# Kernel optimization log

Measured on AMD Instinct MI355X. Metric: run time of the kernel, lower is better.

Reference implementation:

```python
import jax, jax.numpy as jnp
import numpy as np

MARGIN = 0.3
EPS = 1e-12


def setup_inputs() -> dict:
    key = jax.random.key(0)
    k1, k2 = jax.random.split(key)
    inputs = jax.random.normal(k1, (256, 2048), dtype=jnp.float32)
    targets = jax.random.randint(k2, (256,), 0, 32, dtype=jnp.int64)
    return {"inputs": inputs, "targets": targets}


def reference(inputs, targets):
    # Pairwise Euclidean distance matrix [n, n] via GEMM.
    sq = jnp.sum(inputs * inputs, axis=1)                      # [n]
    dist = sq[:, None] + sq[None, :] - 2.0 * (inputs @ inputs.T)
    dist = jnp.sqrt(jnp.clip(dist, EPS, None))                 # [n, n]

    same = targets[:, None] == targets[None, :]                # [n, n]
    # Triplet margin for all (anchor, positive, negative) in one broadcast.
    tri = dist[:, :, None] - dist[:, None, :] + MARGIN         # [n, n, n]
    tri = jnp.clip(tri, EPS, None)
    # Valid: same label for (a, p), different label for (a, neg).
    valid = same[:, :, None] & (~same)[:, None, :]             # [n, n, n]
    # Torch version stacks only valid triplets (dynamic shape); here we
    # return the dense [n, n, n] tensor with invalid entries zeroed.
    return jnp.where(valid, tri, 0.0)
```

## Files before the change

### kernel.cpp

```cpp
#include <hip/hip_runtime.h>
#include <hip/hip_fp16.h>

#define N 256
#define D 2048
#define MARGIN_F 0.3f
#define EPS_F 1e-12f

typedef float v4f __attribute__((ext_vector_type(4)));

__global__ __launch_bounds__(64) void sq_kernel(const float* __restrict__ x,
                                                float* __restrict__ sq) {
    int row = blockIdx.x;
    int lane = threadIdx.x;
    const float4* xr = (const float4*)(x + (size_t)row * D);
    float acc = 0.f;
#pragma unroll
    for (int it = 0; it < 8; ++it) {
        float4 v = xr[lane + 64 * it];
        acc += v.x * v.x + v.y * v.y + v.z * v.z + v.w * v.w;
    }
#pragma unroll
    for (int off = 32; off > 0; off >>= 1) acc += __shfl_down(acc, off, 64);
    if (lane == 0) sq[row] = acc;
}

__global__ __launch_bounds__(256, 1) void gram_kernel(const float* __restrict__ x,
                                                      __half* __restrict__ part) {
    __shared__ __align__(16) float As[128 * 32];
    __shared__ __align__(16) float Bs[128 * 32];
    const int bi = blockIdx.x, bj = blockIdx.y, ks = blockIdx.z;
    const int i0 = bi * 128, j0 = bj * 128, k0 = ks * 32;
    const int tid = threadIdx.x;

#pragma unroll
    for (int it = 0; it < 4; ++it) {
        int f = tid + 256 * it;
        int row = f >> 3;
        int c4 = f & 7;
        int sc4 = c4 ^ ((row >> 3) & 7);
        float4 va = *(const float4*)(x + (size_t)(i0 + row) * D + k0 + c4 * 4);
        float4 vb = *(const float4*)(x + (size_t)(j0 + row) * D + k0 + c4 * 4);
        *(float4*)(As + row * 32 + sc4 * 4) = va;
        *(float4*)(Bs + row * 32 + sc4 * 4) = vb;
    }
    __syncthreads();

    const int tx = tid & 15;
    const int ty = tid >> 4;
    float acc[8][8];
#pragma unroll
    for (int r = 0; r < 8; ++r)
#pragma unroll
        for (int c = 0; c < 8; ++c) acc[r][c] = 0.f;

#pragma unroll
    for (int k4 = 0; k4 < 8; ++k4) {
        float4 a[8], b[8];
#pragma unroll
        for (int r = 0; r < 8; ++r) {
            int ia = ty * 8 + r;
            int ib = tx * 8 + r;
            a[r] = *(const float4*)(As + ia * 32 + ((k4 ^ ((ia >> 3) & 7)) << 2));
            b[r] = *(const float4*)(Bs + ib * 32 + ((k4 ^ ((ib >> 3) & 7)) << 2));
        }
#pragma unroll
        for (int r = 0; r < 8; ++r)
#pragma unroll
            for (int c = 0; c < 8; ++c)
                acc[r][c] += a[r].x * b[c].x + a[r].y * b[c].y +
                             a[r].z * b[c].z + a[r].w * b[c].w;
    }

    __half* pout = part + (size_t)ks * (N * N);
#pragma unroll
    for (int r = 0; r < 8; ++r) {
        int gi = i0 + ty * 8 + r;
        union { __half2 h2[4]; uint4 u; } pk;
#pragma unroll
        for (int c = 0; c < 4; ++c)
            pk.h2[c] = __floats2half2_rn(acc[r][2 * c], acc[r][2 * c + 1]);
        *(uint4*)(pout + (size_t)gi * N + j0 + tx * 8) = pk.u;
    }
}

__global__ __launch_bounds__(256) void fused_kernel(const __half* __restrict__ part,
                                                    const float* __restrict__ sq,
                                                    const int* __restrict__ targets,
                                                    float* __restrict__ out) {
    __shared__ __align__(16) float drow[N];
    __shared__ int lab[N];
    const int a = blockIdx.x;
    const int tid = threadIdx.x;
    lab[tid] = targets[tid];

    float dot = 0.f;
    const __half* base = part + a * N + tid;
#pragma unroll 8
    for (int ks = 0; ks < 64; ++ks)
        dot += __half2float(base[(size_t)ks * (N * N)]);
    drow[tid] = sqrtf(fmaxf(sq[a] + sq[tid] - 2.f * dot, EPS_F));
    __syncthreads();

    const int la = lab[a];
    const int lane = tid & 63;
    const int pq = tid >> 6;
    const int p0 = blockIdx.y * 128 + pq * 32;

    v4f dan = *(const v4f*)(drow + lane * 4);
    v4f mb = MARGIN_F - dan;
    v4f nokv = {(lab[lane * 4 + 0] != la) ? 1.f : 0.f,
                (lab[lane * 4 + 1] != la) ? 1.f : 0.f,
                (lab[lane * 4 + 2] != la) ? 1.f : 0.f,
                (lab[lane * 4 + 3] != la) ? 1.f : 0.f};

    float* obase = out + ((size_t)a << 16) + lane * 4;
#pragma unroll 4
    for (int i = 0; i < 32; ++i) {
        int p = p0 + i;
        v4f r = {0.f, 0.f, 0.f, 0.f};
        if (lab[p] == la) {
            float dap = drow[p];
            v4f t = dap + mb;
            t.x = fmaxf(t.x, EPS_F);
            t.y = fmaxf(t.y, EPS_F);
            t.z = fmaxf(t.z, EPS_F);
            t.w = fmaxf(t.w, EPS_F);
            r = t * nokv;
        }
        __builtin_nontemporal_store(r, (v4f*)(obase + (size_t)p * N));
    }
}

__global__ __launch_bounds__(256) void dist_kernel(const __half* __restrict__ part,
                                                   const float* __restrict__ sq,
                                                   float* __restrict__ dist) {
    const int a = blockIdx.x;
    const int tid = threadIdx.x;
    float dot = 0.f;
    const __half* base = part + a * N + tid;
#pragma unroll 8
    for (int ks = 0; ks < 64; ++ks)
        dot += __half2float(base[(size_t)ks * (N * N)]);
    dist[a * N + tid] = sqrtf(fmaxf(sq[a] + sq[tid] - 2.f * dot, EPS_F));
}

__global__ __launch_bounds__(256) void triplet_kernel(const float* __restrict__ dist,
                                                      const int* __restrict__ targets,
                                                      float* __restrict__ out) {
    __shared__ __align__(16) float drow[N];
    __shared__ int lab[N];
    const int a = blockIdx.x;
    const int p0 = blockIdx.y * 16;
    const int tid = threadIdx.x;
    lab[tid] = targets[tid];
    drow[tid] = dist[a * N + tid];
    __syncthreads();

    const int la = lab[a];
    const int lane = tid & 63;
    const int pq = tid >> 6;

    v4f dan = *(const v4f*)(drow + lane * 4);
    v4f mb = MARGIN_F - dan;
    v4f nokv = {(lab[lane * 4 + 0] != la) ? 1.f : 0.f,
                (lab[lane * 4 + 1] != la) ? 1.f : 0.f,
                (lab[lane * 4 + 2] != la) ? 1.f : 0.f,
                (lab[lane * 4 + 3] != la) ? 1.f : 0.f};

    float* obase = out + ((size_t)a << 16) + lane * 4;
#pragma unroll
    for (int j = 0; j < 4; ++j) {
        int p = p0 + pq * 4 + j;
        v4f r = {0.f, 0.f, 0.f, 0.f};
        if (lab[p] == la) {
            float dap = drow[p];
            v4f t = dap + mb;
            t.x = fmaxf(t.x, EPS_F);
            t.y = fmaxf(t.y, EPS_F);
            t.z = fmaxf(t.z, EPS_F);
            t.w = fmaxf(t.w, EPS_F);
            r = t * nokv;
        }
        __builtin_nontemporal_store(r, (v4f*)(obase + (size_t)p * N));
    }
}

extern "C" void kernel_launch(void* const* d_in, const int* in_sizes, int n_in,
                              void* d_out, int out_size, void* d_ws, size_t ws_size,
                              hipStream_t stream) {
    const float* x = (const float*)d_in[0];
    const int* targets = (const int*)d_in[1];
    float* out = (float*)d_out;
    float* ws = (float*)d_ws;

    float* sq = ws;
    size_t need_full = 1024 + (size_t)64 * N * N * sizeof(__half) + 1024;

    if (ws_size >= need_full) {
        __half* part = (__half*)(ws + 256);
        sq_kernel<<<256, 64, 0, stream>>>(x, sq);
        gram_kernel<<<dim3(2, 2, 64), 256, 0, stream>>>(x, part);
        fused_kernel<<<dim3(256, 2), 256, 0, stream>>>(part, sq, targets, out);
    } else {
        __half* part = (__half*)d_out;
        float* dist = ws + 256;
        sq_kernel<<<256, 64, 0, stream>>>(x, sq);
        gram_kernel<<<dim3(2, 2, 64), 256, 0, stream>>>(x, part);
        dist_kernel<<<256, 256, 0, stream>>>(part, sq, dist);
        triplet_kernel<<<dim3(256, 16), 256, 0, stream>>>(dist, targets, out);
    }
}
```

Before: 95.65 us.

## Retile Gram GEMM to 64x64x64 blocks with 32-way split-K and exact diagonal

The Gram kernel moves from 128x128 output tiles with 32-wide K slices over 64 splits to 64x64 tiles with 64-wide K slices over 32 splits. Shared memory uses a padded stride of 68 with an XOR swizzle, and each thread now holds a 4x4 accumulator instead of 8x8. This raises the block count to 512 and halves the fp16 partial-sum buffer, so the reduction reads half as many partials. The diagonal distance is also fixed to sqrt(eps) to avoid fp16 cancellation error, which is a correctness tweak.

```diff
diff --git a/kernel.cpp b/kernel.cpp
--- a/kernel.cpp
+++ b/kernel.cpp
@@ -5,6 +5,7 @@
 #define D 2048
 #define MARGIN_F 0.3f
 #define EPS_F 1e-12f
+#define SQRT_EPS_F 1e-6f
 
 typedef float v4f __attribute__((ext_vector_type(4)));
 
@@ -24,62 +25,60 @@
     if (lane == 0) sq[row] = acc;
 }
 
-__global__ __launch_bounds__(256, 1) void gram_kernel(const float* __restrict__ x,
-                                                      __half* __restrict__ part) {
-    __shared__ __align__(16) float As[128 * 32];
-    __shared__ __align__(16) float Bs[128 * 32];
-    const int bi = blockIdx.x, bj = blockIdx.y, ks = blockIdx.z;
-    const int i0 = bi * 128, j0 = bj * 128, k0 = ks * 32;
+__global__ __launch_bounds__(256) void gram_kernel(const float* __restrict__ x,
+                                                   __half* __restrict__ part) {
+    __shared__ __align__(16) float As[64 * 68];
+    __shared__ __align__(16) float Bs[64 * 68];
+    const int i0 = blockIdx.x * 64, j0 = blockIdx.y * 64, k0 = blockIdx.z * 64;
     const int tid = threadIdx.x;
 
 #pragma unroll
     for (int it = 0; it < 4; ++it) {
         int f = tid + 256 * it;
-        int row = f >> 3;
-        int c4 = f & 7;
-        int sc4 = c4 ^ ((row >> 3) & 7);
+        int row = f >> 4;
+        int c4 = f & 15;
+        int sc4 = c4 ^ ((row >> 2) & 15);
         float4 va = *(const float4*)(x + (size_t)(i0 + row) * D + k0 + c4 * 4);
         float4 vb = *(const float4*)(x + (size_t)(j0 + row) * D + k0 + c4 * 4);
-        *(float4*)(As + row * 32 + sc4 * 4) = va;
-        *(float4*)(Bs + row * 32 + sc4 * 4) = vb;
+        *(float4*)(As + row * 68 + sc4 * 4) = va;
+        *(float4*)(Bs + row * 68 + sc4 * 4) = vb;
     }
     __syncthreads();
 
     const int tx = tid & 15;
     const int ty = tid >> 4;
-    float acc[8][8];
-#pragma unroll
-    for (int r = 0; r < 8; ++r)
-#pragma unroll
-        for (int c = 0; c < 8; ++c) acc[r][c] = 0.f;
-
-#pragma unroll
-    for (int k4 = 0; k4 < 8; ++k4) {
-        float4 a[8], b[8];
-#pragma unroll
-        for (int r = 0; r < 8; ++r) {
-            int ia = ty * 8 + r;
-            int ib = tx * 8 + r;
-            a[r] = *(const float4*)(As + ia * 32 + ((k4 ^ ((ia >> 3) & 7)) << 2));
-            b[r] = *(const float4*)(Bs + ib * 32 + ((k4 ^ ((ib >> 3) & 7)) << 2));
+    float acc[4][4];
+#pragma unroll
+    for (int r = 0; r < 4; ++r)
+#pragma unroll
+        for (int c = 0; c < 4; ++c) acc[r][c] = 0.f;
+
+#pragma unroll
+    for (int k4 = 0; k4 < 16; ++k4) {
+        float4 a[4], b[4];
+        const int ca = (k4 ^ ty) << 2;
+        const int cb = (k4 ^ tx) << 2;
+#pragma unroll
+        for (int r = 0; r < 4; ++r) {
+            a[r] = *(const float4*)(As + (ty * 4 + r) * 68 + ca);
+            b[r] = *(const float4*)(Bs + (tx * 4 + r) * 68 + cb);
         }
 #pragma unroll
-        for (int r = 0; r < 8; ++r)
-#pragma unroll
-            for (int c = 0; c < 8; ++c)
+        for (int r = 0; r < 4; ++r)
+#pragma unroll
+            for (int c = 0; c < 4; ++c)
                 acc[r][c] += a[r].x * b[c].x + a[r].y * b[c].y +
                              a[r].z * b[c].z + a[r].w * b[c].w;
     }
 
-    __half* pout = part + (size_t)ks * (N * N);
-#pragma unroll
-    for (int r = 0; r < 8; ++r) {
-        int gi = i0 + ty * 8 + r;
-        union { __half2 h2[4]; uint4 u; } pk;
-#pragma unroll
-        for (int c = 0; c < 4; ++c)
-            pk.h2[c] = __floats2half2_rn(acc[r][2 * c], acc[r][2 * c + 1]);
-        *(uint4*)(pout + (size_t)gi * N + j0 + tx * 8) = pk.u;
+    __half* pout = part + (size_t)blockIdx.z * (N * N);
+#pragma unroll
+    for (int r = 0; r < 4; ++r) {
+        int gi = i0 + ty * 4 + r;
+        union { __half2 h2[2]; uint2 u; } pk;
+        pk.h2[0] = __floats2half2_rn(acc[r][0], acc[r][1]);
+        pk.h2[1] = __floats2half2_rn(acc[r][2], acc[r][3]);
+        *(uint2*)(pout + (size_t)gi * N + j0 + tx * 4) = pk.u;
     }
 }
 
@@ -96,9 +95,10 @@
     float dot = 0.f;
     const __half* base = part + a * N + tid;
 #pragma unroll 8
-    for (int ks = 0; ks < 64; ++ks)
+    for (int ks = 0; ks < 32; ++ks)
         dot += __half2float(base[(size_t)ks * (N * N)]);
-    drow[tid] = sqrtf(fmaxf(sq[a] + sq[tid] - 2.f * dot, EPS_F));
+    drow[tid] = (tid == a) ? SQRT_EPS_F
+                           : sqrtf(fmaxf(sq[a] + sq[tid] - 2.f * dot, EPS_F));
     __syncthreads();
 
     const int la = lab[a];
@@ -139,9 +139,10 @@
     float dot = 0.f;
     const __half* base = part + a * N + tid;
 #pragma unroll 8
-    for (int ks = 0; ks < 64; ++ks)
+    for (int ks = 0; ks < 32; ++ks)
         dot += __half2float(base[(size_t)ks * (N * N)]);
-    dist[a * N + tid] = sqrtf(fmaxf(sq[a] + sq[tid] - 2.f * dot, EPS_F));
+    dist[a * N + tid] = (tid == a) ? SQRT_EPS_F
+                                   : sqrtf(fmaxf(sq[a] + sq[tid] - 2.f * dot, EPS_F));
 }
 
 __global__ __launch_bounds__(256) void triplet_kernel(const float* __restrict__ dist,
@@ -194,18 +195,18 @@
     float* ws = (float*)d_ws;
 
     float* sq = ws;
-    size_t need_full = 1024 + (size_t)64 * N * N * sizeof(__half) + 1024;
+    size_t need_full = 1024 + (size_t)32 * N * N * sizeof(__half) + 1024;
 
     if (ws_size >= need_full) {
         __half* part = (__half*)(ws + 256);
         sq_kernel<<<256, 64, 0, stream>>>(x, sq);
-        gram_kernel<<<dim3(2, 2, 64), 256, 0, stream>>>(x, part);
+        gram_kernel<<<dim3(4, 4, 32), 256, 0, stream>>>(x, part);
         fused_kernel<<<dim3(256, 2), 256, 0, stream>>>(part, sq, targets, out);
     } else {
         __half* part = (__half*)d_out;
         float* dist = ws + 256;
         sq_kernel<<<256, 64, 0, stream>>>(x, sq);
-        gram_kernel<<<dim3(2, 2, 64), 256, 0, stream>>>(x, part);
+        gram_kernel<<<dim3(4, 4, 32), 256, 0, stream>>>(x, part);
         dist_kernel<<<256, 256, 0, stream>>>(part, sq, dist);
         triplet_kernel<<<dim3(256, 16), 256, 0, stream>>>(dist, targets, out);
     }
```

Result: faster. 92.46 us (-3.3%).
